# Kernel tuning notes

Measured on AMD Instinct MI355X. Metric: run time of the kernel, lower is better.

Reference implementation:

```python
import jax, jax.numpy as jnp
import numpy as np

N_NODES = 100000
N_EDGES = 1600000
NFEAT, NHID1, NCLASS = 256, 128, 64
NUM_GRAPHS = 64


def gcn_conv(x, edge_index, edge_weight, W, b):
    # PyG GCNConv: linear transform, add self-loops (weight 1), symmetric norm, scatter-add
    n = x.shape[0]
    x = x @ W  # [N, out]
    loop = jnp.arange(n)
    row = jnp.concatenate([edge_index[0], loop])  # source
    col = jnp.concatenate([edge_index[1], loop])  # target
    w = jnp.concatenate([edge_weight, jnp.ones((n,), dtype=x.dtype)])
    deg = jax.ops.segment_sum(w, col, num_segments=n)
    dinv = jnp.where(deg > 0, jax.lax.rsqrt(jnp.maximum(deg, 1e-30)), 0.0)
    norm = dinv[row] * w * dinv[col]  # [E+N]
    out = jax.ops.segment_sum(x[row] * norm[:, None], col, num_segments=n)
    return out + b


def setup_inputs() -> dict:
    key = jax.random.key(0)
    ks = jax.random.split(key, 12)
    x = jax.random.normal(ks[0], (N_NODES, NFEAT), dtype=jnp.float32)
    edge_index = jax.random.randint(ks[1], (2, N_EDGES), 0, N_NODES, dtype=jnp.int64)
    edge_weight = jax.random.uniform(ks[2], (N_EDGES,), dtype=jnp.float32)
    batch = jnp.sort(jax.random.randint(ks[3], (N_NODES,), 0, NUM_GRAPHS, dtype=jnp.int64))
    def glorot(k, shape):
        lim = float(np.sqrt(6.0 / (shape[0] + shape[1])))
        return jax.random.uniform(k, shape, jnp.float32, -lim, lim)
    W1 = glorot(ks[4], (NFEAT, NHID1)); b1 = jnp.zeros((NHID1,), jnp.float32)
    W2 = glorot(ks[5], (NHID1, NCLASS)); b2 = jnp.zeros((NCLASS,), jnp.float32)
    l1w = glorot(ks[6], (NCLASS, 64)); l1b = jnp.zeros((64,), jnp.float32)
    l2w = glorot(ks[7], (64, 2)); l2b = jnp.zeros((2,), jnp.float32)
    return {"x": x, "edge_index": edge_index, "edge_weight": edge_weight, "batch": batch,
            "W1": W1, "b1": b1, "W2": W2, "b2": b2,
            "l1w": l1w, "l1b": l1b, "l2w": l2w, "l2b": l2b}


def reference(x, edge_index, edge_weight, batch, W1, b1, W2, b2, l1w, l1b, l2w, l2b):
    h = jax.nn.relu(gcn_conv(x, edge_index, edge_weight, W1, b1))
    h = jax.nn.relu(gcn_conv(h, edge_index, edge_weight, W2, b2))
    pooled = jax.ops.segment_sum(h, batch, num_segments=NUM_GRAPHS)  # global_add_pool
    h = jax.nn.relu(pooled @ l1w + l1b)
    out = h @ l2w + l2b
    Y_prob = jax.nn.log_softmax(out, axis=1)
    Y_hat = jnp.argmax(Y_prob, axis=1).astype(jnp.float32)
    return (Y_prob, Y_hat, out)
```

## Files before the change

kernel.cpp:

```cpp
#include <hip/hip_runtime.h>
#include <hip/hip_bf16.h>
#include <math.h>

#define N_NODES 100000
#define N_EDGES 1600000
#define NFEAT 256
#define NHID1 128
#define NCLASS 64
#define NUM_GRAPHS 64

#define NBUCK 391
#define EPB 8192
#define NBLK_A 196

typedef __attribute__((ext_vector_type(8))) short bf16x8;
typedef __attribute__((ext_vector_type(4))) float f32x4;


__device__ __forceinline__ unsigned short f2bf(float f) {
    unsigned u = __float_as_uint(f);
    u += 0x7fffu + ((u >> 16) & 1u);
    return (unsigned short)(u >> 16);
}
__device__ __forceinline__ unsigned packbf2(float lo, float hi) {
    return (unsigned)f2bf(lo) | ((unsigned)f2bf(hi) << 16);
}
__device__ __forceinline__ float bflo(unsigned p) { return __uint_as_float(p << 16); }
__device__ __forceinline__ float bfhi(unsigned p) { return __uint_as_float(p & 0xffff0000u); }

template <int LU>
__device__ __forceinline__ void ldrow(unsigned* dst, const unsigned* p) {
    if constexpr (LU == 4) {
        uint4 v = *(const uint4*)p;
        dst[0] = v.x; dst[1] = v.y; dst[2] = v.z; dst[3] = v.w;
    } else {
        uint2 v = *(const uint2*)p;
        dst[0] = v.x; dst[1] = v.y;
    }
}

template <int LU>
__device__ __forceinline__ void accum(float* acc, const unsigned* p, float w) {
    #pragma unroll
    for (int u = 0; u < LU; u++) {
        acc[2 * u]     += bflo(p[u]) * w;
        acc[2 * u + 1] += bfhi(p[u]) * w;
    }
}


__global__ __launch_bounds__(256) void hist_rank_kernel(const int* __restrict__ cols,
                                                        int* __restrict__ ghist,
                                                        unsigned short* __restrict__ rk,
                                                        int* __restrict__ hbk, int nE) {
    __shared__ int h[NBUCK];
    const int tid = threadIdx.x;
    for (int i = tid; i < NBUCK; i += 256) h[i] = 0;
    __syncthreads();
    long base = (long)blockIdx.x * EPB;
    for (int j = tid; j < EPB; j += 256) {
        long idx = base + j;
        if (idx < nE) rk[idx] = (unsigned short)atomicAdd(&h[cols[idx] >> 8], 1);
    }
    __syncthreads();
    int* hrow = hbk + blockIdx.x * NBUCK;
    for (int i = tid; i < NBUCK; i += 256) {
        int v = h[i];
        hrow[i] = v;
        if (v) atomicAdd(&ghist[i], v);
    }
}


__global__ __launch_bounds__(512) void bucket_scan_kernel(const int* __restrict__ ghist,
                                                          int* __restrict__ gbase,
                                                          int* __restrict__ gcursor) {
    __shared__ int sh[512];
    int t = threadIdx.x;
    int v = (t < NBUCK) ? ghist[t] : 0;
    sh[t] = v;
    __syncthreads();
    for (int off = 1; off < 512; off <<= 1) {
        int add = (t >= off) ? sh[t - off] : 0;
        __syncthreads();
        sh[t] += add;
        __syncthreads();
    }
    if (t < NBUCK) {
        int excl = sh[t] - v;
        gbase[t] = excl;
        gcursor[t] = excl;
    }
}


__global__ __launch_bounds__(256) void scatter_bucket_kernel(const int* __restrict__ rows,
                                                             const int* __restrict__ cols,
                                                             const float* __restrict__ w,
                                                             int* __restrict__ gcursor,
                                                             const int* __restrict__ hbk,
                                                             const unsigned short* __restrict__ rk,
                                                             int2* __restrict__ csc_tmp, int nE) {
    __shared__ int bb[NBUCK];
    const int tid = threadIdx.x;
    const int* hrow = hbk + blockIdx.x * NBUCK;
    for (int i = tid; i < NBUCK; i += 256) {
        int v = hrow[i];
        bb[i] = v ? atomicAdd(&gcursor[i], v) : 0;
    }
    __syncthreads();
    long base = (long)blockIdx.x * EPB;
    for (int j = tid; j < EPB; j += 256) {
        long idx = base + j;
        if (idx < nE) {
            int c = cols[idx];
            int b = c >> 8;
            int pos = bb[b] + (int)rk[idx];
            csc_tmp[pos] = make_int2((rows[idx] & 0x1FFFF) | ((c & 255) << 17),
                                     __float_as_int(w[idx]));
        }
    }
}


__global__ __launch_bounds__(256) void build_csc_kernel(const int2* __restrict__ csc_tmp,
                                                        const int* __restrict__ gbase,
                                                        const int* __restrict__ ghist,
                                                        int2* __restrict__ edges,
                                                        int* __restrict__ starts,
                                                        int* __restrict__ cnt,
                                                        float* __restrict__ dinv, int n) {
    __shared__ int ncnt[256];
    __shared__ float nws[256];
    __shared__ int sh[256];
    __shared__ int ncur[256];
    const int tid = threadIdx.x;
    const int b = blockIdx.x;
    const int base = gbase[b];
    const int cntb = ghist[b];

    ncnt[tid] = 0;
    nws[tid] = 0.f;
    __syncthreads();

    for (int i = tid; i < cntb; i += 256) {
        int2 rec = csc_tmp[base + i];
        int local = ((unsigned)rec.x) >> 17;
        atomicAdd(&ncnt[local], 1);
        atomicAdd(&nws[local], __int_as_float(rec.y));
    }
    __syncthreads();

    int v = ncnt[tid];
    sh[tid] = v;
    __syncthreads();
    for (int off = 1; off < 256; off <<= 1) {
        int add = (tid >= off) ? sh[tid - off] : 0;
        __syncthreads();
        sh[tid] += add;
        __syncthreads();
    }
    int excl = sh[tid] - v;
    ncur[tid] = excl;

    int node = (b << 8) + tid;
    if (node < n) {
        cnt[node] = v;
        starts[node] = base + excl;
        dinv[node] = rsqrtf(1.0f + nws[tid]);
    }
    __syncthreads();

    for (int i = tid; i < cntb; i += 256) {
        int2 rec = csc_tmp[base + i];
        int local = ((unsigned)rec.x) >> 17;
        int r = rec.x & 0x1FFFF;
        int pos = base + atomicAdd(&ncur[local], 1);
        edges[pos] = make_int2(r, rec.y);
    }
}


__global__ void transpose_bf_kernel(const float* __restrict__ W, unsigned* __restrict__ WT,
                                    int K, int Nn) {
    int idx = blockIdx.x * blockDim.x + threadIdx.x;
    int total = Nn * (K / 2);
    if (idx < total) {
        int n = idx / (K / 2);
        int kp = idx - n * (K / 2);
        WT[idx] = packbf2(W[(2 * kp) * Nn + n], W[(2 * kp + 1) * Nn + n]);
    }
}


template <int NT, int KK, bool ABF16>
__global__ __launch_bounds__(256) void gemm_mfma(const void* __restrict__ Av,
                                                 const unsigned* __restrict__ BT,
                                                 const float* __restrict__ rowscale,
                                                 unsigned short* __restrict__ C,
                                                 int M) {
    constexpr int CT = NT / 16;
    constexpr int KD = KK / 2;
    __shared__ unsigned Al[4][128][4];
    __shared__ unsigned Bl[4][NT][4];
    const int tid = threadIdx.x;
    const int wave = tid >> 6;
    const int lane = tid & 63;
    const int quad = lane >> 4;
    const int l16 = lane & 15;
    const int row0 = blockIdx.x * 128;

    f32x4 acc[2][CT] = {};

    for (int k0 = 0; k0 < KK; k0 += 32) {
        if (ABF16) {
            const unsigned* Ab = (const unsigned*)Av;
            #pragma unroll
            for (int i = 0; i < 2; i++) {
                int idx = tid + i * 256;
                int ar = idx >> 2, aq = idx & 3;
                uint4 v = make_uint4(0, 0, 0, 0);
                if (row0 + ar < M)
                    v = *(const uint4*)(Ab + (long)(row0 + ar) * KD + k0 / 2 + aq * 4);
                *(uint4*)&Al[aq][ar][0] = v;
            }
        } else {
            const float* Af = (const float*)Av;
            int ar = tid >> 1, ah = tid & 1;
            float4 v0 = make_float4(0, 0, 0, 0), v1 = v0, v2 = v0, v3 = v0;
            if (row0 + ar < M) {
                const float* p = Af + (long)(row0 + ar) * KK + k0 + ah * 16;
                v0 = *(const float4*)p;
                v1 = *(const float4*)(p + 4);
                v2 = *(const float4*)(p + 8);
                v3 = *(const float4*)(p + 12);
            }
            uint4 d0 = make_uint4(packbf2(v0.x, v0.y), packbf2(v0.z, v0.w),
                                  packbf2(v1.x, v1.y), packbf2(v1.z, v1.w));
            uint4 d1 = make_uint4(packbf2(v2.x, v2.y), packbf2(v2.z, v2.w),
                                  packbf2(v3.x, v3.y), packbf2(v3.z, v3.w));
            *(uint4*)&Al[ah * 2 + 0][ar][0] = d0;
            *(uint4*)&Al[ah * 2 + 1][ar][0] = d1;
        }
        #pragma unroll
        for (int i = 0; i < NT / 64; i++) {
            int idx = tid + i * 256;
            int br = idx >> 2, bq = idx & 3;
            *(uint4*)&Bl[bq][br][0] = *(const uint4*)(BT + (long)br * KD + k0 / 2 + bq * 4);
        }
        __syncthreads();

        bf16x8 af[2];
        #pragma unroll
        for (int rt = 0; rt < 2; rt++)
            af[rt] = *(const bf16x8*)&Al[quad][wave * 32 + rt * 16 + l16][0];
        #pragma unroll
        for (int ct = 0; ct < CT; ct++) {
            bf16x8 bfr = *(const bf16x8*)&Bl[quad][ct * 16 + l16][0];
            acc[0][ct] = __builtin_amdgcn_mfma_f32_16x16x32_bf16(af[0], bfr, acc[0][ct], 0, 0, 0);
            acc[1][ct] = __builtin_amdgcn_mfma_f32_16x16x32_bf16(af[1], bfr, acc[1][ct], 0, 0, 0);
        }
        __syncthreads();
    }

    #pragma unroll
    for (int rt = 0; rt < 2; rt++) {
        #pragma unroll
        for (int reg = 0; reg < 4; reg++) {
            int row = row0 + wave * 32 + rt * 16 + quad * 4 + reg;
            if (row < M) {
                float sc = rowscale[row];
                unsigned short* cp = C + (long)row * NT + l16;
                #pragma unroll
                for (int ct = 0; ct < CT; ct++)
                    cp[ct * 16] = f2bf(acc[rt][ct][reg] * sc);
            }
        }
    }
}


template <int F, int FPL, bool RELU, int OUTMODE>
__global__ __launch_bounds__(256) void gather_agg_bf(const unsigned* __restrict__ xsb,
                                                     const int2* __restrict__ edges,
                                                     const int* __restrict__ starts,
                                                     const int* __restrict__ cnt,
                                                     const float* __restrict__ dinv,
                                                     const float* __restrict__ bias,
                                                     const int* __restrict__ batch,
                                                     void* __restrict__ outv, int n) {
    constexpr int G = F / FPL;
    constexpr int FU = F / 2;
    constexpr int LU = FPL / 2;
    int gt = blockIdx.x * blockDim.x + threadIdx.x;
    int node = gt / G;
    int lane = gt - node * G;

    if (OUTMODE != 2 && node >= n) return;
    bool active = (node < n);

    __shared__ float lp[4][64];
    int g0 = 0;
    if (OUTMODE == 2) {
        lp[threadIdx.x >> 6][threadIdx.x & 63] = 0.f;
        int firstnode = (blockIdx.x * blockDim.x) / G;
        if (firstnode >= n) firstnode = n - 1;
        g0 = batch[firstnode];
        __syncthreads();
    }

    float acc[FPL] = {};
    float d = 0.f;
    const unsigned* lbase = xsb + lane * LU;
    unsigned sp[LU] = {};
    float bbv[FPL] = {};

    if (active) {
        d = dinv[node];
        ldrow<LU>(sp, lbase + (long)node * FU);
        if constexpr (FPL == 8) {
            float4 bb0 = ((const float4*)bias)[lane * 2];
            float4 bb1 = ((const float4*)bias)[lane * 2 + 1];
            bbv[0] = bb0.x; bbv[1] = bb0.y; bbv[2] = bb0.z; bbv[3] = bb0.w;
            bbv[4] = bb1.x; bbv[5] = bb1.y; bbv[6] = bb1.z; bbv[7] = bb1.w;
        } else {
            float4 bb0 = ((const float4*)bias)[lane];
            bbv[0] = bb0.x; bbv[1] = bb0.y; bbv[2] = bb0.z; bbv[3] = bb0.w;
        }

        int s = starts[node];
        int c = cnt[node];
        int e = s + c;
        int j = s;

        long long q0 = 0, q1 = 0, q2 = 0, q3 = 0;
        bool have = (j + 4 <= e);
        if (have) {
            const long long* ep = (const long long*)(edges + j);
            q0 = ep[0]; q1 = ep[1]; q2 = ep[2]; q3 = ep[3];
            j += 4;
        }
        while (have) {
            int r0 = (int)q0, r1 = (int)q1, r2 = (int)q2, r3 = (int)q3;
            float w0 = __int_as_float((int)(q0 >> 32));
            float w1 = __int_as_float((int)(q1 >> 32));
            float w2 = __int_as_float((int)(q2 >> 32));
            float w3 = __int_as_float((int)(q3 >> 32));
            unsigned p0[LU], p1[LU], p2[LU], p3[LU];
            ldrow<LU>(p0, lbase + (long)r0 * FU);
            ldrow<LU>(p1, lbase + (long)r1 * FU);
            ldrow<LU>(p2, lbase + (long)r2 * FU);
            ldrow<LU>(p3, lbase + (long)r3 * FU);
            have = (j + 4 <= e);
            if (have) {
                const long long* ep = (const long long*)(edges + j);
                q0 = ep[0]; q1 = ep[1]; q2 = ep[2]; q3 = ep[3];
                j += 4;
            }
            accum<LU>(acc, p0, w0);
            accum<LU>(acc, p1, w1);
            accum<LU>(acc, p2, w2);
            accum<LU>(acc, p3, w3);
        }
        for (; j < e; j++) {
            int2 ed = edges[j];
            float wv = __int_as_float(ed.y);
            unsigned p[LU];
            ldrow<LU>(p, lbase + (long)ed.x * FU);
            accum<LU>(acc, p, wv);
        }
    }

    float r[FPL] = {};
    if (active) {
        #pragma unroll
        for (int u = 0; u < LU; u++) {
            float slo = bflo(sp[u]), shi = bfhi(sp[u]);
            float v0 = d * (acc[2 * u] + slo) + bbv[2 * u];
            float v1 = d * (acc[2 * u + 1] + shi) + bbv[2 * u + 1];
            r[2 * u]     = RELU ? fmaxf(v0, 0.f) : v0;
            r[2 * u + 1] = RELU ? fmaxf(v1, 0.f) : v1;
        }
    }

    if (OUTMODE == 1) {
        if (active) {
            unsigned* ob = (unsigned*)outv;
            if constexpr (FPL == 8) {
                uint4 pk = make_uint4(packbf2(r[0], r[1]), packbf2(r[2], r[3]),
                                      packbf2(r[4], r[5]), packbf2(r[6], r[7]));
                *(uint4*)(ob + (long)node * FU + lane * LU) = pk;
            } else {
                uint2 pk = make_uint2(packbf2(r[0], r[1]), packbf2(r[2], r[3]));
                *(uint2*)(ob + (long)node * FU + lane * LU) = pk;
            }
        }
    } else if (OUTMODE == 0) {
        if (active) {
            float* o = (float*)outv + (long)node * F + lane * FPL;
            #pragma unroll
            for (int i = 0; i < FPL; i++) o[i] = r[i];
        }
    } else {
        float* pooled = (float*)outv;
        if (active) {
            int g = batch[node];
            int rel = g - g0;
            if (rel >= 0 && rel < 4) {
                #pragma unroll
                for (int i = 0; i < FPL; i++)
                    atomicAdd(&lp[rel][lane * FPL + i], r[i]);
            } else {
                #pragma unroll
                for (int i = 0; i < FPL; i++)
                    atomicAdd(&pooled[g * 64 + lane * FPL + i], r[i]);
            }
        }
        __syncthreads();
        int idx = threadIdx.x;
        int rel = idx >> 6, feat = idx & 63;
        float v = lp[rel][feat];
        int g = g0 + rel;
        if (v != 0.f && g < NUM_GRAPHS)
            atomicAdd(&pooled[g * 64 + feat], v);
    }
}


__global__ __launch_bounds__(256) void head_kernel(const float* __restrict__ pooled,
                                                   const float* __restrict__ l1w,
                                                   const float* __restrict__ l1b,
                                                   const float* __restrict__ l2w,
                                                   const float* __restrict__ l2b,
                                                   float* __restrict__ out) {
    __shared__ float P[64][68];
    __shared__ float W[64][68];
    __shared__ float red0[64][4];
    __shared__ float red1[64][4];
    const int tid = threadIdx.x;

    for (int i = tid; i < 1024; i += 256) {
        int r = i >> 4;
        int cq = (i & 15) * 4;
        *(float4*)&P[r][cq] = *(const float4*)&pooled[r * 64 + cq];
        *(float4*)&W[r][cq] = *(const float4*)&l1w[r * 64 + cq];
    }
    __syncthreads();

    const int g = tid >> 2;
    const int q = tid & 3;
    const int j0 = q * 16;

    float hacc[16];
    #pragma unroll
    for (int jj = 0; jj < 16; jj++) hacc[jj] = l1b[j0 + jj];

    for (int c = 0; c < 64; c++) {
        float pv = P[g][c];
        #pragma unroll
        for (int jj = 0; jj < 16; jj += 4) {
            float4 wv = *(const float4*)&W[c][j0 + jj];
            hacc[jj + 0] += pv * wv.x;
            hacc[jj + 1] += pv * wv.y;
            hacc[jj + 2] += pv * wv.z;
            hacc[jj + 3] += pv * wv.w;
        }
    }

    float o0 = 0.f, o1 = 0.f;
    #pragma unroll
    for (int jj = 0; jj < 16; jj++) {
        float h = fmaxf(hacc[jj], 0.f);
        o0 += h * l2w[(j0 + jj) * 2];
        o1 += h * l2w[(j0 + jj) * 2 + 1];
    }
    red0[g][q] = o0;
    red1[g][q] = o1;
    __syncthreads();

    if (q == 0) {
        float a0 = red0[g][0] + red0[g][1] + red0[g][2] + red0[g][3] + l2b[0];
        float a1 = red1[g][0] + red1[g][1] + red1[g][2] + red1[g][3] + l2b[1];
        float m = fmaxf(a0, a1);
        float lse = m + logf(expf(a0 - m) + expf(a1 - m));
        out[g * 2 + 0] = a0 - lse;
        out[g * 2 + 1] = a1 - lse;
        out[128 + g] = (a1 > a0) ? 1.f : 0.f;
        out[192 + g * 2 + 0] = a0;
        out[192 + g * 2 + 1] = a1;
    }
}


extern "C" void kernel_launch(void* const* d_in, const int* in_sizes, int n_in,
                              void* d_out, int out_size, void* d_ws, size_t ws_size,
                              hipStream_t stream) {
    const float* x   = (const float*)d_in[0];
    const int* eidx  = (const int*)d_in[1];
    const float* ew  = (const float*)d_in[2];
    const int* batch = (const int*)d_in[3];
    const float* W1  = (const float*)d_in[4];
    const float* b1  = (const float*)d_in[5];
    const float* W2  = (const float*)d_in[6];
    const float* b2  = (const float*)d_in[7];
    const float* l1w = (const float*)d_in[8];
    const float* l1b = (const float*)d_in[9];
    const float* l2w = (const float*)d_in[10];
    const float* l2b = (const float*)d_in[11];
    float* out = (float*)d_out;

    const int N = N_NODES, E = N_EDGES;
    const int* rows = eidx;
    const int* cols = eidx + E;

    float* ws = (float*)d_ws;
    int*   ghist   = (int*)ws;
    int*   gbase   = ghist + 512;
    int*   gcursor = gbase + 512;
    float* dinv    = (float*)(gcursor + 512);
    int*   cnt     = (int*)(dinv + N);
    int*   starts  = cnt + N;
    unsigned* w1t  = (unsigned*)(starts + N);
    unsigned* w2t  = w1t + 16384;
    int2*  csc_tmp = (int2*)(w2t + 4096);
    int2*  edges   = csc_tmp + E;
    unsigned* xsb  = (unsigned*)(edges + E);
    unsigned* h1b  = xsb + (long)N * 64;
    float* pooled  = (float*)(h1b + (long)N * 64);
    unsigned* hw2b = xsb;
    unsigned short* rk = (unsigned short*)edges;
    int* hbk = (int*)xsb;

    hipMemsetAsync(ghist, 0, 512 * sizeof(int), stream);
    hist_rank_kernel<<<NBLK_A, 256, 0, stream>>>(cols, ghist, rk, hbk, E);

    bucket_scan_kernel<<<1, 512, 0, stream>>>(ghist, gbase, gcursor);

    scatter_bucket_kernel<<<NBLK_A, 256, 0, stream>>>(rows, cols, ew, gcursor, hbk, rk, csc_tmp, E);

    build_csc_kernel<<<NBUCK, 256, 0, stream>>>(csc_tmp, gbase, ghist, edges, starts, cnt, dinv, N);

    transpose_bf_kernel<<<64, 256, 0, stream>>>(W1, w1t, NFEAT, NHID1);
    transpose_bf_kernel<<<16, 256, 0, stream>>>(W2, w2t, NHID1, NCLASS);

    gemm_mfma<NHID1, NFEAT, false><<<(N + 127) / 128, 256, 0, stream>>>(
        x, w1t, dinv, (unsigned short*)xsb, N);

    {
        long threads = (long)N * (NHID1 / 8);
        gather_agg_bf<NHID1, 8, true, 1><<<(threads + 255) / 256, 256, 0, stream>>>(
            xsb, edges, starts, cnt, dinv, b1, batch, h1b, N);
    }

    gemm_mfma<NCLASS, NHID1, true><<<(N + 127) / 128, 256, 0, stream>>>(
        h1b, w2t, dinv, (unsigned short*)hw2b, N);

    hipMemsetAsync(pooled, 0, NUM_GRAPHS * NCLASS * sizeof(float), stream);
    {
        long threads = (long)N * (NCLASS / 4);
        gather_agg_bf<NCLASS, 4, true, 2><<<(threads + 255) / 256, 256, 0, stream>>>(
            hw2b, edges, starts, cnt, dinv, b2, batch, pooled, N);
    }

    head_kernel<<<1, 256, 0, stream>>>(pooled, l1w, l1b, l2w, l2b, out);
}
```

Baseline: 419.3 us.

## Replace two-pass bucketed CSC build with global-atomic degree count and scatter

The CSC build now counts per-node degree and weight sum with global atomics, runs a per-bucket scan to get node starts, then scatters edges directly with per-node atomic cursors. This drops the two-level bucket scatter, the temporary buffer and the rank array. The gather loop is also unrolled to eight edges per batch with a predicated tail, and layer 2 switches to eight features per lane. The global atomics contend on hot nodes, and the intra-node edge order becomes nondeterministic, which can change float summation order.

```diff
diff --git a/kernel.cpp b/kernel.cpp
--- a/kernel.cpp
+++ b/kernel.cpp
@@ -49,10 +49,11 @@
 }
 
 
-__global__ __launch_bounds__(256) void hist_rank_kernel(const int* __restrict__ cols,
-                                                        int* __restrict__ ghist,
-                                                        unsigned short* __restrict__ rk,
-                                                        int* __restrict__ hbk, int nE) {
+__global__ __launch_bounds__(256) void hist_deg_kernel(const int* __restrict__ cols,
+                                                       const float* __restrict__ ew,
+                                                       int* __restrict__ ghist,
+                                                       int* __restrict__ cnt,
+                                                       float* __restrict__ wsum, int nE) {
     __shared__ int h[NBUCK];
     const int tid = threadIdx.x;
     for (int i = tid; i < NBUCK; i += 256) h[i] = 0;
@@ -60,21 +61,23 @@
     long base = (long)blockIdx.x * EPB;
     for (int j = tid; j < EPB; j += 256) {
         long idx = base + j;
-        if (idx < nE) rk[idx] = (unsigned short)atomicAdd(&h[cols[idx] >> 8], 1);
+        if (idx < nE) {
+            int c = cols[idx];
+            atomicAdd(&h[c >> 8], 1);
+            atomicAdd(&cnt[c], 1);
+            atomicAdd(&wsum[c], ew[idx]);
+        }
     }
     __syncthreads();
-    int* hrow = hbk + blockIdx.x * NBUCK;
     for (int i = tid; i < NBUCK; i += 256) {
         int v = h[i];
-        hrow[i] = v;
         if (v) atomicAdd(&ghist[i], v);
     }
 }
 
 
 __global__ __launch_bounds__(512) void bucket_scan_kernel(const int* __restrict__ ghist,
-                                                          int* __restrict__ gbase,
-                                                          int* __restrict__ gcursor) {
+                                                          int* __restrict__ gbase) {
     __shared__ int sh[512];
     int t = threadIdx.x;
     int v = (t < NBUCK) ? ghist[t] : 0;
@@ -86,72 +89,21 @@
         sh[t] += add;
         __syncthreads();
     }
-    if (t < NBUCK) {
-        int excl = sh[t] - v;
-        gbase[t] = excl;
-        gcursor[t] = excl;
-    }
-}
-
-
-__global__ __launch_bounds__(256) void scatter_bucket_kernel(const int* __restrict__ rows,
-                                                             const int* __restrict__ cols,
-                                                             const float* __restrict__ w,
-                                                             int* __restrict__ gcursor,
-                                                             const int* __restrict__ hbk,
-                                                             const unsigned short* __restrict__ rk,
-                                                             int2* __restrict__ csc_tmp, int nE) {
-    __shared__ int bb[NBUCK];
-    const int tid = threadIdx.x;
-    const int* hrow = hbk + blockIdx.x * NBUCK;
-    for (int i = tid; i < NBUCK; i += 256) {
-        int v = hrow[i];
-        bb[i] = v ? atomicAdd(&gcursor[i], v) : 0;
-    }
-    __syncthreads();
-    long base = (long)blockIdx.x * EPB;
-    for (int j = tid; j < EPB; j += 256) {
-        long idx = base + j;
-        if (idx < nE) {
-            int c = cols[idx];
-            int b = c >> 8;
-            int pos = bb[b] + (int)rk[idx];
-            csc_tmp[pos] = make_int2((rows[idx] & 0x1FFFF) | ((c & 255) << 17),
-                                     __float_as_int(w[idx]));
-        }
-    }
-}
-
-
-__global__ __launch_bounds__(256) void build_csc_kernel(const int2* __restrict__ csc_tmp,
-                                                        const int* __restrict__ gbase,
-                                                        const int* __restrict__ ghist,
-                                                        int2* __restrict__ edges,
+    if (t < NBUCK) gbase[t] = sh[t] - v;
+}
+
+
+__global__ __launch_bounds__(256) void node_scan_kernel(const int* __restrict__ gbase,
+                                                        const int* __restrict__ cnt,
+                                                        const float* __restrict__ wsum,
                                                         int* __restrict__ starts,
-                                                        int* __restrict__ cnt,
+                                                        int* __restrict__ ncur,
                                                         float* __restrict__ dinv, int n) {
-    __shared__ int ncnt[256];
-    __shared__ float nws[256];
     __shared__ int sh[256];
-    __shared__ int ncur[256];
     const int tid = threadIdx.x;
     const int b = blockIdx.x;
-    const int base = gbase[b];
-    const int cntb = ghist[b];
-
-    ncnt[tid] = 0;
-    nws[tid] = 0.f;
-    __syncthreads();
-
-    for (int i = tid; i < cntb; i += 256) {
-        int2 rec = csc_tmp[base + i];
-        int local = ((unsigned)rec.x) >> 17;
-        atomicAdd(&ncnt[local], 1);
-        atomicAdd(&nws[local], __int_as_float(rec.y));
-    }
-    __syncthreads();
-
-    int v = ncnt[tid];
+    int node = (b << 8) + tid;
+    int v = (node < n) ? cnt[node] : 0;
     sh[tid] = v;
     __syncthreads();
     for (int off = 1; off < 256; off <<= 1) {
@@ -160,23 +112,24 @@
         sh[tid] += add;
         __syncthreads();
     }
-    int excl = sh[tid] - v;
-    ncur[tid] = excl;
-
-    int node = (b << 8) + tid;
     if (node < n) {
-        cnt[node] = v;
-        starts[node] = base + excl;
-        dinv[node] = rsqrtf(1.0f + nws[tid]);
-    }
-    __syncthreads();
-
-    for (int i = tid; i < cntb; i += 256) {
-        int2 rec = csc_tmp[base + i];
-        int local = ((unsigned)rec.x) >> 17;
-        int r = rec.x & 0x1FFFF;
-        int pos = base + atomicAdd(&ncur[local], 1);
-        edges[pos] = make_int2(r, rec.y);
+        int st = gbase[b] + sh[tid] - v;
+        starts[node] = st;
+        ncur[node] = st;
+        dinv[node] = rsqrtf(1.0f + wsum[node]);
+    }
+}
+
+
+__global__ __launch_bounds__(256) void scatter_final_kernel(const int* __restrict__ rows,
+                                                            const int* __restrict__ cols,
+                                                            const float* __restrict__ ew,
+                                                            int* __restrict__ ncur,
+                                                            int2* __restrict__ edges, int nE) {
+    int idx = blockIdx.x * 256 + threadIdx.x;
+    if (idx < nE) {
+        int pos = atomicAdd(&ncur[cols[idx]], 1);
+        edges[pos] = make_int2(rows[idx], __float_as_int(ew[idx]));
     }
 }
 
@@ -331,43 +284,65 @@
         int s = starts[node];
         int c = cnt[node];
         int e = s + c;
-        int j = s;
-
-        long long q0 = 0, q1 = 0, q2 = 0, q3 = 0;
-        bool have = (j + 4 <= e);
-        if (have) {
-            const long long* ep = (const long long*)(edges + j);
+        int eM = s + ((c >> 3) << 3);
+
+        long long q0 = 0, q1 = 0, q2 = 0, q3 = 0, q4 = 0, q5 = 0, q6 = 0, q7 = 0;
+        int jb = s;
+        if (jb < eM) {
+            const long long* ep = (const long long*)(edges + jb);
             q0 = ep[0]; q1 = ep[1]; q2 = ep[2]; q3 = ep[3];
-            j += 4;
-        }
-        while (have) {
+            q4 = ep[4]; q5 = ep[5]; q6 = ep[6]; q7 = ep[7];
+        }
+        while (jb < eM) {
             int r0 = (int)q0, r1 = (int)q1, r2 = (int)q2, r3 = (int)q3;
+            int r4 = (int)q4, r5 = (int)q5, r6 = (int)q6, r7 = (int)q7;
             float w0 = __int_as_float((int)(q0 >> 32));
             float w1 = __int_as_float((int)(q1 >> 32));
             float w2 = __int_as_float((int)(q2 >> 32));
             float w3 = __int_as_float((int)(q3 >> 32));
-            unsigned p0[LU], p1[LU], p2[LU], p3[LU];
+            float w4 = __int_as_float((int)(q4 >> 32));
+            float w5 = __int_as_float((int)(q5 >> 32));
+            float w6 = __int_as_float((int)(q6 >> 32));
+            float w7 = __int_as_float((int)(q7 >> 32));
+            unsigned p0[LU], p1[LU], p2[LU], p3[LU], p4[LU], p5[LU], p6[LU], p7[LU];
             ldrow<LU>(p0, lbase + (long)r0 * FU);
             ldrow<LU>(p1, lbase + (long)r1 * FU);
             ldrow<LU>(p2, lbase + (long)r2 * FU);
             ldrow<LU>(p3, lbase + (long)r3 * FU);
-            have = (j + 4 <= e);
-            if (have) {
-                const long long* ep = (const long long*)(edges + j);
+            ldrow<LU>(p4, lbase + (long)r4 * FU);
+            ldrow<LU>(p5, lbase + (long)r5 * FU);
+            ldrow<LU>(p6, lbase + (long)r6 * FU);
+            ldrow<LU>(p7, lbase + (long)r7 * FU);
+            jb += 8;
+            if (jb < eM) {
+                const long long* ep = (const long long*)(edges + jb);
                 q0 = ep[0]; q1 = ep[1]; q2 = ep[2]; q3 = ep[3];
-                j += 4;
+                q4 = ep[4]; q5 = ep[5]; q6 = ep[6]; q7 = ep[7];
             }
             accum<LU>(acc, p0, w0);
             accum<LU>(acc, p1, w1);
             accum<LU>(acc, p2, w2);
             accum<LU>(acc, p3, w3);
-        }
-        for (; j < e; j++) {
-            int2 ed = edges[j];
-            float wv = __int_as_float(ed.y);
-            unsigned p[LU];
-            ldrow<LU>(p, lbase + (long)ed.x * FU);
-            accum<LU>(acc, p, wv);
+            accum<LU>(acc, p4, w4);
+            accum<LU>(acc, p5, w5);
+            accum<LU>(acc, p6, w6);
+            accum<LU>(acc, p7, w7);
+        }
+
+        if (eM < e) {
+            long long qt[7];
+            #pragma unroll
+            for (int t = 0; t < 7; t++)
+                qt[t] = (eM + t < e) ? *(const long long*)(edges + eM + t) : 0;
+            #pragma unroll
+            for (int t = 0; t < 7; t++) {
+                if (eM + t < e) {
+                    float wv = __int_as_float((int)(qt[t] >> 32));
+                    unsigned p[LU];
+                    ldrow<LU>(p, lbase + (long)((int)qt[t]) * FU);
+                    accum<LU>(acc, p, wv);
+                }
+            }
         }
     }
 
@@ -516,29 +491,28 @@
     float* ws = (float*)d_ws;
     int*   ghist   = (int*)ws;
     int*   gbase   = ghist + 512;
-    int*   gcursor = gbase + 512;
-    float* dinv    = (float*)(gcursor + 512);
-    int*   cnt     = (int*)(dinv + N);
-    int*   starts  = cnt + N;
-    unsigned* w1t  = (unsigned*)(starts + N);
+    float* dinv    = (float*)(gbase + 512);
+    int*   starts  = (int*)(dinv + N);
+    int*   cnt     = starts + N;
+    float* wsum    = (float*)(cnt + N);
+    int*   ncur    = (int*)(wsum + N);
+    unsigned* w1t  = (unsigned*)(ncur + N);
     unsigned* w2t  = w1t + 16384;
-    int2*  csc_tmp = (int2*)(w2t + 4096);
-    int2*  edges   = csc_tmp + E;
+    int2*  edges   = (int2*)(w2t + 4096);
     unsigned* xsb  = (unsigned*)(edges + E);
     unsigned* h1b  = xsb + (long)N * 64;
     float* pooled  = (float*)(h1b + (long)N * 64);
     unsigned* hw2b = xsb;
-    unsigned short* rk = (unsigned short*)edges;
-    int* hbk = (int*)xsb;
 
     hipMemsetAsync(ghist, 0, 512 * sizeof(int), stream);
-    hist_rank_kernel<<<NBLK_A, 256, 0, stream>>>(cols, ghist, rk, hbk, E);
-
-    bucket_scan_kernel<<<1, 512, 0, stream>>>(ghist, gbase, gcursor);
-
-    scatter_bucket_kernel<<<NBLK_A, 256, 0, stream>>>(rows, cols, ew, gcursor, hbk, rk, csc_tmp, E);
-
-    build_csc_kernel<<<NBUCK, 256, 0, stream>>>(csc_tmp, gbase, ghist, edges, starts, cnt, dinv, N);
+    hipMemsetAsync(cnt, 0, 2 * N * sizeof(int), stream);
+    hist_deg_kernel<<<NBLK_A, 256, 0, stream>>>(cols, ew, ghist, cnt, wsum, E);
+
+    bucket_scan_kernel<<<1, 512, 0, stream>>>(ghist, gbase);
+
+    node_scan_kernel<<<NBUCK, 256, 0, stream>>>(gbase, cnt, wsum, starts, ncur, dinv, N);
+
+    scatter_final_kernel<<<(E + 255) / 256, 256, 0, stream>>>(rows, cols, ew, ncur, edges, E);
 
     transpose_bf_kernel<<<64, 256, 0, stream>>>(W1, w1t, NFEAT, NHID1);
     transpose_bf_kernel<<<16, 256, 0, stream>>>(W2, w2t, NHID1, NCLASS);
@@ -557,8 +531,8 @@
 
     hipMemsetAsync(pooled, 0, NUM_GRAPHS * NCLASS * sizeof(float), stream);
     {
-        long threads = (long)N * (NCLASS / 4);
-        gather_agg_bf<NCLASS, 4, true, 2><<<(threads + 255) / 256, 256, 0, stream>>>(
+        long threads = (long)N * (NCLASS / 8);
+        gather_agg_bf<NCLASS, 8, true, 2><<<(threads + 255) / 256, 256, 0, stream>>>(
             hw2b, edges, starts, cnt, dinv, b2, batch, pooled, N);
     }
 
```

Measured after the change: 616.5 us. 1.47x slower.
